# Performance work log

Hardware: AMD Instinct MI355X
Metric: run time of the kernel (lower is better)

The kernel has to match this reference:

```python
import jax, jax.numpy as jnp
import numpy as np

B, N, C, H = 8, 1024, 768, 12
D = C // H
HID = 4 * C
MAX_TEXT_LEN = 512
LN_EPS = 1e-5


def _ln(x, g, b):
    mu = jnp.mean(x, axis=-1, keepdims=True)
    var = jnp.mean(jnp.square(x - mu), axis=-1, keepdims=True)
    return (x - mu) * jax.lax.rsqrt(var + LN_EPS) * g + b


def _mlp(x, w1, b1, w2, b2):
    h = jax.nn.gelu(x @ w1.T + b1, approximate=False)
    return h @ w2.T + b2


def setup_inputs() -> dict:
    key = jax.random.key(0)
    ks = jax.random.split(key, 16)
    s = 0.02
    return {
        "x": jax.random.normal(ks[0], (B, N, C), jnp.float32),
        "mask": jax.random.randint(ks[1], (B, N), 0, 2).astype(bool),
        "rel_bias": jax.random.normal(ks[2], (H, N, N), jnp.float32) * s,
        "w_qkv": jax.random.normal(ks[3], (3 * C, C), jnp.float32) * s,
        "q_bias": jnp.zeros((C,), jnp.float32),
        "v_bias": jnp.zeros((C,), jnp.float32),
        "w_proj": jax.random.normal(ks[4], (C, C), jnp.float32) * s,
        "b_proj": jnp.zeros((C,), jnp.float32),
        "ln1_g": jnp.ones((C,), jnp.float32),
        "ln1_b": jnp.zeros((C,), jnp.float32),
        "ln2t_g": jnp.ones((C,), jnp.float32),
        "ln2t_b": jnp.zeros((C,), jnp.float32),
        "ln2i_g": jnp.ones((C,), jnp.float32),
        "ln2i_b": jnp.zeros((C,), jnp.float32),
        "w1t": jax.random.normal(ks[5], (HID, C), jnp.float32) * s,
        "b1t": jnp.zeros((HID,), jnp.float32),
        "w2t": jax.random.normal(ks[6], (C, HID), jnp.float32) * s,
        "b2t": jnp.zeros((C,), jnp.float32),
        "w1i": jax.random.normal(ks[7], (HID, C), jnp.float32) * s,
        "b1i": jnp.zeros((HID,), jnp.float32),
        "w2i": jax.random.normal(ks[8], (C, HID), jnp.float32) * s,
        "b2i": jnp.zeros((C,), jnp.float32),
        "gamma1": jnp.full((C,), 0.1, jnp.float32),
        "gamma2": jnp.full((C,), 0.1, jnp.float32),
    }


def reference(x, mask, rel_bias, w_qkv, q_bias, v_bias, w_proj, b_proj,
              ln1_g, ln1_b, ln2t_g, ln2t_b, ln2i_g, ln2i_b,
              w1t, b1t, w2t, b2t, w1i, b1i, w2i, b2i, gamma1, gamma2):
    # ---- attention branch ----
    h = _ln(x, ln1_g, ln1_b)
    qkv_bias = jnp.concatenate([q_bias, jnp.zeros_like(v_bias), v_bias])
    qkv = h @ w_qkv.T + qkv_bias                      # [B,N,3C]
    qkv = qkv.reshape(B, N, 3, H, D).transpose(2, 0, 3, 1, 4)  # [3,B,H,N,D]
    q, k, v = qkv[0], qkv[1], qkv[2]
    q = q * (D ** -0.5)
    attn = jnp.einsum('bhnd,bhmd->bhnm',
                      q.astype(jnp.float32), k.astype(jnp.float32))
    attn = attn + rel_bias[None]                      # [B,H,N,N]
    attn = jnp.where(mask[:, None, None, :], attn, -jnp.inf)
    attn = jax.nn.softmax(attn, axis=-1).astype(x.dtype)
    out = jnp.einsum('bhnm,bhmd->bhnd', attn, v)
    out = out.transpose(0, 2, 1, 3).reshape(B, N, C)
    out = out @ w_proj.T + b_proj
    x = x + gamma1 * out
    # ---- dual-branch layer-scaled MLP (mlp_vl is None path) ----
    xt = x[:, :MAX_TEXT_LEN]
    xi = x[:, MAX_TEXT_LEN:]
    xt = xt + gamma2 * _mlp(_ln(xt, ln2t_g, ln2t_b), w1t, b1t, w2t, b2t)
    xi = xi + gamma2 * _mlp(_ln(xi, ln2i_g, ln2i_b), w1i, b1i, w2i, b2i)
    return jnp.concatenate([xt, xi], axis=1)
```

## Files before the change

### kernel.cpp

```cpp
#include <hip/hip_runtime.h>
#include <hip/hip_bf16.h>
#include <math.h>

#define B_    8
#define N_TOK 1024
#define C_    768
#define H_    12
#define D_    64
#define HID_  3072

typedef __attribute__((ext_vector_type(4)))  float f32x4;
typedef __attribute__((ext_vector_type(16))) float f32x16;
typedef __attribute__((ext_vector_type(8)))  short s16x8;
typedef __attribute__((ext_vector_type(4)))  unsigned short u16x4;

static __device__ __forceinline__ unsigned short f2bf(float x){
  union { __hip_bfloat16 h; unsigned short u; } cv;
  cv.h = __float2bfloat16(x);
  return cv.u;
}
static __device__ __forceinline__ float bf2f(unsigned short u){
  return __uint_as_float(((unsigned)u) << 16);
}

#define GLOAD_LDS16(gp, lp) \
  __builtin_amdgcn_global_load_lds((const __attribute__((address_space(1))) unsigned int*)(gp), \
                                   (__attribute__((address_space(3))) unsigned int*)(lp), 16, 0, 0)

__global__ __launch_bounds__(256) void k_cvtall(
    const float* __restrict__ wq,  const float* __restrict__ wp,
    const float* __restrict__ w1t, const float* __restrict__ w2t,
    const float* __restrict__ w1i, const float* __restrict__ w2i,
    const float* __restrict__ bias,
    unsigned short* __restrict__ dq,  unsigned short* __restrict__ dp,
    unsigned short* __restrict__ d1t, unsigned short* __restrict__ d2t,
    unsigned short* __restrict__ d1i, unsigned short* __restrict__ d2i,
    unsigned short* __restrict__ db)
{
  int i = blockIdx.x * 256 + threadIdx.x;
  const float* src; unsigned short* dst; int o;
  if      (i <  442368){ src = wq;  dst = dq;  o = i; }
  else if (i <  589824){ src = wp;  dst = dp;  o = i -  442368; }
  else if (i < 1179648){ src = w1t; dst = d1t; o = i -  589824; }
  else if (i < 1769472){ src = w2t; dst = d2t; o = i - 1179648; }
  else if (i < 2359296){ src = w1i; dst = d1i; o = i - 1769472; }
  else if (i < 2949120){ src = w2i; dst = d2i; o = i - 2359296; }
  else                 { src = bias;dst = db;  o = i - 2949120; }
  float4 v = ((const float4*)src)[o];
  u16x4 r;
  r.x = f2bf(v.x); r.y = f2bf(v.y); r.z = f2bf(v.z); r.w = f2bf(v.w);
  *(u16x4*)(dst + (size_t)o*4) = r;
}

__global__ __launch_bounds__(256) void k_ln1(const float* __restrict__ x,
                                             const float* __restrict__ g,
                                             const float* __restrict__ bta,
                                             unsigned short* __restrict__ out){
  int row  = blockIdx.x*4 + (threadIdx.x >> 6);
  int lane = threadIdx.x & 63;
  const float* xr = x + (size_t)row*C_;
  float v[12]; float s = 0.f;
  #pragma unroll
  for (int i=0;i<12;i++){ v[i] = xr[lane + i*64]; s += v[i]; }
  #pragma unroll
  for (int m=1;m<64;m<<=1) s += __shfl_xor(s, m);
  float mu = s * (1.f/768.f);
  float vs = 0.f;
  #pragma unroll
  for (int i=0;i<12;i++){ float d = v[i]-mu; vs += d*d; }
  #pragma unroll
  for (int m=1;m<64;m<<=1) vs += __shfl_xor(vs, m);
  float rs = rsqrtf(vs*(1.f/768.f) + 1e-5f);
  unsigned short* orow = out + (size_t)row*C_;
  #pragma unroll
  for (int i=0;i<12;i++){ int c = lane + i*64; orow[c] = f2bf((v[i]-mu)*rs*g[c] + bta[c]); }
}

__global__ __launch_bounds__(256) void k_ln2(const float* __restrict__ xmid,
                                             const float* __restrict__ gt, const float* __restrict__ bt,
                                             const float* __restrict__ gi, const float* __restrict__ bi,
                                             unsigned short* __restrict__ outc){
  int row  = blockIdx.x*4 + (threadIdx.x >> 6);
  int lane = threadIdx.x & 63;
  int bb = row >> 10, n = row & 1023;
  const float* G = (n < 512) ? gt : gi;
  const float* Bb = (n < 512) ? bt : bi;
  int crow = (n < 512) ? (bb*512 + n) : (4096 + bb*512 + (n - 512));
  const float* xr = xmid + (size_t)row*C_;
  float v[12]; float s = 0.f;
  #pragma unroll
  for (int i=0;i<12;i++){ v[i] = xr[lane + i*64]; s += v[i]; }
  #pragma unroll
  for (int m=1;m<64;m<<=1) s += __shfl_xor(s, m);
  float mu = s * (1.f/768.f);
  float vs = 0.f;
  #pragma unroll
  for (int i=0;i<12;i++){ float d = v[i]-mu; vs += d*d; }
  #pragma unroll
  for (int m=1;m<64;m<<=1) vs += __shfl_xor(vs, m);
  float rs = rsqrtf(vs*(1.f/768.f) + 1e-5f);
  unsigned short* orow = outc + (size_t)crow*C_;
  #pragma unroll
  for (int i=0;i<12;i++){ int c = lane + i*64; orow[c] = f2bf((v[i]-mu)*rs*G[c] + Bb[c]); }
}

template<int MODE, int TM>
__global__ __launch_bounds__(TM==256 ? 512 : 256, TM==256 ? 2 : 3) void k_gemm2(
    const unsigned short* __restrict__ A,
    const unsigned short* __restrict__ Bw0,
    const unsigned short* __restrict__ Bw1,
    int K,
    const float* __restrict__ bias0,
    const float* __restrict__ bias1,
    const float* __restrict__ qb2,
    const float* __restrict__ resid,
    const float* __restrict__ gamma,
    unsigned short* __restrict__ out_bf,
    float* __restrict__ out_f)
{
  constexpr int THREADS = (TM == 256) ? 512 : 256;
  constexpr int ASLOT = TM * 64;
  constexpr int SLOT  = ASLOT + 8192;
  constexpr int BITS  = 8192 / (THREADS * 16);
  __shared__ __align__(16) char smem[3 * SLOT];
  const int tid = threadIdx.x;
  const int lane = tid & 63, w = tid >> 6;
  const int wr = w >> 1, wc = w & 1;
  const int l31 = lane & 31, h5 = lane >> 5;

  const int gx = gridDim.x, gy = gridDim.y;
  const int nwg = gx * gy;
  const int flat = blockIdx.y * gx + blockIdx.x;
  const int nid = (flat & 7) * (nwg >> 3) + (flat >> 3);
  const int by = nid % gy, bx = nid / gy;
  const int z = blockIdx.z;
  const int row0 = bx*TM, col0 = by*128;

  const unsigned short* Ap = A;
  const unsigned short* Bp = Bw0;
  const float* bias = bias0;
  if (MODE == 2 || MODE == 3){
    if (z){ Ap = A + (size_t)4096*K; Bp = Bw1; bias = bias1; }
  }
  const char* Abase = (const char*)Ap;
  const char* Bbase = (const char*)Bp;
  const size_t rowbytes = (size_t)K*2;
  const int KT2 = K >> 5;

  auto stage = [&](int h, int slot_idx){
    char* slot = smem + slot_idx*SLOT;
    size_t kb = (size_t)h*64;
    #pragma unroll
    for (int it = 0; it < 2; it++){
      int L = it*(THREADS*16) + tid*16;
      int r = L >> 6, cb = L & 63;
      GLOAD_LDS16(Abase + (size_t)(row0 + r)*rowbytes + kb + (cb ^ ((r & 6) << 3)), slot + L);
    }
    #pragma unroll
    for (int it = 0; it < BITS; it++){
      int L = it*(THREADS*16) + tid*16;
      int r = L >> 6, cb = L & 63;
      GLOAD_LDS16(Bbase + (size_t)(col0 + r)*rowbytes + kb + (cb ^ ((r & 6) << 3)), slot + ASLOT + L);
    }
  };

  stage(0, 0); stage(1, 1);
  if constexpr (TM == 256) asm volatile("s_waitcnt vmcnt(3)" ::: "memory");
  else                     asm volatile("s_waitcnt vmcnt(4)" ::: "memory");
  __builtin_amdgcn_s_barrier();

  f32x16 acc[2][2] = {};
  int sh = 2, sc_ = 0;
  for (int h = 0; h < KT2; h++){
    if (h + 2 < KT2){
      stage(h + 2, sh);
      sh = (sh == 2) ? 0 : sh + 1;
    }
    char* slot = smem + sc_*SLOT;
    sc_ = (sc_ == 2) ? 0 : sc_ + 1;
    s16x8 af[2][2], bfr[2][2];
    #pragma unroll
    for (int fm = 0; fm < 2; fm++){
      int ra = wr*64 + fm*32 + l31;
      int swa = (ra & 6) << 3;
      af[fm][0] = *(const s16x8*)(slot + ra*64 + ((h5*16) ^ swa));
      af[fm][1] = *(const s16x8*)(slot + ra*64 + ((32 + h5*16) ^ swa));
    }
    #pragma unroll
    for (int fn = 0; fn < 2; fn++){
      int rb = wc*64 + fn*32 + l31;
      int swb = (rb & 6) << 3;
      bfr[fn][0] = *(const s16x8*)(slot + ASLOT + rb*64 + ((h5*16) ^ swb));
      bfr[fn][1] = *(const s16x8*)(slot + ASLOT + rb*64 + ((32 + h5*16) ^ swb));
    }
    __builtin_amdgcn_s_setprio(1);
    #pragma unroll
    for (int kh = 0; kh < 2; kh++)
      #pragma unroll
      for (int fm = 0; fm < 2; fm++)
        #pragma unroll
        for (int fn = 0; fn < 2; fn++)
          acc[fm][fn] = __builtin_amdgcn_mfma_f32_32x32x16_bf16(af[fm][kh], bfr[fn][kh], acc[fm][fn], 0, 0, 0);
    __builtin_amdgcn_s_setprio(0);
    if (h + 1 < KT2){
      if (h + 2 < KT2){
        if constexpr (TM == 256) asm volatile("s_waitcnt vmcnt(3)" ::: "memory");
        else                     asm volatile("s_waitcnt vmcnt(4)" ::: "memory");
      } else {
        asm volatile("s_waitcnt vmcnt(0)" ::: "memory");
      }
      __builtin_amdgcn_s_barrier();
    }
  }

  #pragma unroll
  for (int fm = 0; fm < 2; fm++){
    #pragma unroll
    for (int fn = 0; fn < 2; fn++){
      int j = col0 + wc*64 + fn*32 + l31;
      f32x16 a = acc[fm][fn];
      if (MODE == 0){
        int which = (j >= 1536) ? 2 : (j >= 768 ? 1 : 0);
        int cj = j - which*768;
        float bs = (which == 0) ? bias0[cj] : (which == 2 ? qb2[cj] : 0.f);
        int head = cj >> 6, d = cj & 63;
        #pragma unroll
        for (int r = 0; r < 16; r++){
          int m = row0 + wr*64 + fm*32 + (r & 3) + 8*(r >> 2) + 4*h5;
          int bb = m >> 10, n = m & 1023;
          float val = a[r] + bs;
          if (which == 0) val *= 0.125f;
          out_bf[((((size_t)which*B_ + bb)*H_ + head)*N_TOK + n)*D_ + d] = f2bf(val);
        }
      } else if (MODE == 1){
        float gm = gamma[j], bs = bias[j];
        #pragma unroll
        for (int r = 0; r < 16; r++){
          int m = row0 + wr*64 + fm*32 + (r & 3) + 8*(r >> 2) + 4*h5;
          size_t idx = (size_t)m*C_ + j;
          out_f[idx] = resid[idx] + gm*(a[r] + bs);
        }
      } else if (MODE == 2){
        float bs = bias[j];
        unsigned short* outp = out_bf + (size_t)z*4096*HID_;
        #pragma unroll
        for (int r = 0; r < 16; r++){
          int m = row0 + wr*64 + fm*32 + (r & 3) + 8*(r >> 2) + 4*h5;
          float t = a[r] + bs;
          outp[(size_t)m*HID_ + j] = f2bf(0.5f*t*(1.f + erff(t*0.70710678118654752f)));
        }
      } else {
        float gm = gamma[j], bs = bias[j];
        #pragma unroll
        for (int r = 0; r < 16; r++){
          int m = row0 + wr*64 + fm*32 + (r & 3) + 8*(r >> 2) + 4*h5;
          int bb = m >> 9, n = (m & 511) + (z ? 512 : 0);
          size_t idx = ((size_t)bb*N_TOK + n)*C_ + j;
          out_f[idx] = resid[idx] + gm*(a[r] + bs);
        }
      }
    }
  }
}

__global__ __launch_bounds__(256, 2) void k_attn(
    const unsigned short* __restrict__ qb,
    const unsigned short* __restrict__ kb,
    const unsigned short* __restrict__ vb,
    const unsigned short* __restrict__ bias_bf,
    const int* __restrict__ mask,
    unsigned short* __restrict__ outb)
{
  __shared__ __align__(16) char smem[45056];
  char* Vt0 = smem;
  char* Vt1 = smem + 8192;
  char* Ks  = smem + 16384;
  char* Bs  = smem + 24576;
  float* maskf = (float*)(smem + 40960);
  char* Oep = smem;

  int wg = blockIdx.x;
  int x = wg & 7, rest = wg >> 3;
  int qt = rest & 7, gl = rest >> 3;
  int g = gl*8 + x;
  int h = g % 12, bb = g / 12;

  const int tid = threadIdx.x, lane = tid & 63, w = tid >> 6;
  const int l31 = lane & 31, h5 = lane >> 5;
  const size_t bh = (size_t)bb*H_ + h;
  const char* qp = (const char*)(qb + bh*N_TOK*D_);
  const char* kp = (const char*)(kb + bh*N_TOK*D_);
  const unsigned short* vp = vb + bh*N_TOK*D_;
  const char* bp = (const char*)(bias_bf + (size_t)h*N_TOK*N_TOK);
  const int q0 = qt*128;
  const int qrow = q0 + w*32 + l31;
  const int qr = w*32 + l31;

  #pragma unroll
  for (int it = 0; it < 2; it++){
    int L = it*4096 + tid*16; int r = L >> 7, cb = L & 127;
    GLOAD_LDS16(kp + (size_t)r*128 + (cb ^ ((r & 7) << 4)), Ks + L);
  }
  #pragma unroll
  for (int it = 0; it < 4; it++){
    int L = it*4096 + tid*16; int r = L >> 7, cb = L & 127;
    GLOAD_LDS16(bp + (size_t)(q0 + r)*2048 + (cb ^ ((r & 7) << 4)), Bs + L);
  }
  unsigned short vv[16];
  #pragma unroll
  for (int j = 0; j < 16; j++) vv[j] = vp[(size_t)(w*16 + j)*D_ + lane];
  {
    int4 m4 = *(const int4*)(mask + bb*N_TOK + tid*4);
    float4 f4;
    f4.x = m4.x ? 0.f : -1e30f; f4.y = m4.y ? 0.f : -1e30f;
    f4.z = m4.z ? 0.f : -1e30f; f4.w = m4.w ? 0.f : -1e30f;
    *(float4*)(maskf + tid*4) = f4;
  }
  s16x8 qf[4];
  #pragma unroll
  for (int t = 0; t < 4; t++)
    qf[t] = *(const s16x8*)(qp + (size_t)qrow*128 + t*32 + h5*16);
  #pragma unroll
  for (int i = 0; i < 2; i++){
    s16x8 pk;
    #pragma unroll
    for (int e = 0; e < 8; e++) pk[e] = (short)vv[i*8 + e];
    *(s16x8*)(Vt0 + lane*128 + ((w*32 + i*16) ^ ((lane & 7) << 4))) = pk;
  }
  __syncthreads();

  f32x16 oacc[2] = {};
  float lrow = 0.f;

  for (int t = 0; t < 16; t++){
    const int kt = t*64;
    char* Vbuf = (t & 1) ? Vt1 : Vt0;
    char* Vnxt = (t & 1) ? Vt0 : Vt1;

    s16x8 kfr[2][4];
    #pragma unroll
    for (int ck = 0; ck < 2; ck++)
      #pragma unroll
      for (int tt = 0; tt < 4; tt++)
        kfr[ck][tt] = *(const s16x8*)(Ks + (ck*32 + l31)*128 + ((tt*32 + h5*16) ^ ((l31 & 7) << 4)));
    u16x4 bv[2][4];
    #pragma unroll
    for (int ck = 0; ck < 2; ck++)
      #pragma unroll
      for (int rq = 0; rq < 4; rq++){
        int off = ck*64 + rq*16 + h5*8;
        bv[ck][rq] = *(const u16x4*)(Bs + qr*128 + (off ^ ((qr & 7) << 4)));
      }
    __syncthreads();

    if (t < 15){
      #pragma unroll
      for (int it = 0; it < 2; it++){
        int L = it*4096 + tid*16; int r = L >> 7, cb = L & 127;
        GLOAD_LDS16(kp + (size_t)(kt + 64 + r)*128 + (cb ^ ((r & 7) << 4)), Ks + L);
      }
      #pragma unroll
      for (int it = 0; it < 4; it++){
        int L = it*4096 + tid*16; int r = L >> 7, cb = L & 127;
        GLOAD_LDS16(bp + (size_t)(q0 + r)*2048 + (size_t)(kt + 64)*2 + (cb ^ ((r & 7) << 4)), Bs + L);
      }
      #pragma unroll
      for (int j = 0; j < 16; j++)
        vv[j] = vp[(size_t)(kt + 64 + w*16 + j)*D_ + lane];
    }

    f32x16 sacc[2] = {};
    __builtin_amdgcn_s_setprio(1);
    #pragma unroll
    for (int tt = 0; tt < 4; tt++){
      sacc[0] = __builtin_amdgcn_mfma_f32_32x32x16_bf16(kfr[0][tt], qf[tt], sacc[0], 0, 0, 0);
      sacc[1] = __builtin_amdgcn_mfma_f32_32x32x16_bf16(kfr[1][tt], qf[tt], sacc[1], 0, 0, 0);
    }
    __builtin_amdgcn_s_setprio(0);

    float sv[2][16];
    float ps = 0.f;
    #pragma unroll
    for (int ck = 0; ck < 2; ck++){
      #pragma unroll
      for (int r = 0; r < 16; r++){
        int kk = ck*32 + (r & 3) + 8*(r >> 2) + 4*h5;
        float p = __expf(sacc[ck][r] + bf2f(bv[ck][r >> 2][r & 3]) + maskf[kt + kk]);
        sv[ck][r] = p;
        ps += p;
      }
    }
    lrow += ps;

    #pragma unroll
    for (int ck = 0; ck < 2; ck++){
      #pragma unroll
      for (int kh = 0; kh < 2; kh++){
        unsigned wA, wB, wC, wD;
        asm("v_cvt_pk_bf16_f32 %0, %1, %2" : "=v"(wA) : "v"(sv[ck][kh*8+0]), "v"(sv[ck][kh*8+1]));
        asm("v_cvt_pk_bf16_f32 %0, %1, %2" : "=v"(wB) : "v"(sv[ck][kh*8+2]), "v"(sv[ck][kh*8+3]));
        asm("v_cvt_pk_bf16_f32 %0, %1, %2" : "=v"(wC) : "v"(sv[ck][kh*8+4]), "v"(sv[ck][kh*8+5]));
        asm("v_cvt_pk_bf16_f32 %0, %1, %2" : "=v"(wD) : "v"(sv[ck][kh*8+6]), "v"(sv[ck][kh*8+7]));
        unsigned tA = (unsigned)__shfl_xor((int)wA, 32);
        unsigned tB = (unsigned)__shfl_xor((int)wB, 32);
        unsigned tC = (unsigned)__shfl_xor((int)wC, 32);
        unsigned tD = (unsigned)__shfl_xor((int)wD, 32);
        union { unsigned u[4]; s16x8 v; } pu;
        pu.u[0] = h5 ? tC : wA;
        pu.u[1] = h5 ? tD : wB;
        pu.u[2] = h5 ? wC : tA;
        pu.u[3] = h5 ? wD : tB;
        __builtin_amdgcn_s_setprio(1);
        #pragma unroll
        for (int dt = 0; dt < 2; dt++){
          int d = dt*32 + l31;
          s16x8 vf = *(const s16x8*)(Vbuf + d*128 + ((ck*64 + kh*32 + h5*16) ^ ((d & 7) << 4)));
          oacc[dt] = __builtin_amdgcn_mfma_f32_32x32x16_bf16(vf, pu.v, oacc[dt], 0, 0, 0);
        }
        __builtin_amdgcn_s_setprio(0);
      }
    }

    if (t < 15){
      #pragma unroll
      for (int i = 0; i < 2; i++){
        s16x8 pk;
        #pragma unroll
        for (int e = 0; e < 8; e++) pk[e] = (short)vv[i*8 + e];
        *(s16x8*)(Vnxt + lane*128 + ((w*32 + i*16) ^ ((lane & 7) << 4))) = pk;
      }
    }
    __syncthreads();
  }

  lrow += __shfl_xor(lrow, 32);
  float inv = 1.f / lrow;
  char* Ow = Oep + w*8192;
  #pragma unroll
  for (int dt = 0; dt < 2; dt++)
    #pragma unroll
    for (int r = 0; r < 16; r++){
      int d = dt*32 + (r & 3) + 8*(r >> 2) + 4*h5;
      *(float*)(Ow + l31*256 + ((d*4) ^ ((l31 & 7) << 4))) = oacc[dt][r] * inv;
    }
  int q2 = lane >> 1, dh = lane & 1;
  float of[32];
  #pragma unroll
  for (int i = 0; i < 8; i++){
    f32x4 v4 = *(const f32x4*)(Ow + q2*256 + ((dh*128 + i*16) ^ ((q2 & 7) << 4)));
    of[i*4+0] = v4[0]; of[i*4+1] = v4[1]; of[i*4+2] = v4[2]; of[i*4+3] = v4[3];
  }
  unsigned short* orow = outb + ((size_t)bb*N_TOK + q0 + w*32 + q2)*C_ + h*64 + dh*32;
  #pragma unroll
  for (int i = 0; i < 4; i++){
    s16x8 ob;
    #pragma unroll
    for (int e = 0; e < 8; e++) ob[e] = (short)f2bf(of[i*8+e]);
    *(s16x8*)(orow + i*8) = ob;
  }
}

extern "C" void kernel_launch(void* const* d_in, const int* in_sizes, int n_in,
                              void* d_out, int out_size, void* d_ws, size_t ws_size,
                              hipStream_t stream) {
  const float* x      = (const float*)d_in[0];
  const int*   mask   = (const int*)  d_in[1];
  const float* relb   = (const float*)d_in[2];
  const float* w_qkv  = (const float*)d_in[3];
  const float* q_bias = (const float*)d_in[4];
  const float* v_bias = (const float*)d_in[5];
  const float* w_proj = (const float*)d_in[6];
  const float* b_proj = (const float*)d_in[7];
  const float* ln1_g  = (const float*)d_in[8];
  const float* ln1_b  = (const float*)d_in[9];
  const float* ln2t_g = (const float*)d_in[10];
  const float* ln2t_b = (const float*)d_in[11];
  const float* ln2i_g = (const float*)d_in[12];
  const float* ln2i_b = (const float*)d_in[13];
  const float* w1t    = (const float*)d_in[14];
  const float* b1t    = (const float*)d_in[15];
  const float* w2t    = (const float*)d_in[16];
  const float* b2t    = (const float*)d_in[17];
  const float* w1i    = (const float*)d_in[18];
  const float* b1i    = (const float*)d_in[19];
  const float* w2i    = (const float*)d_in[20];
  const float* b2i    = (const float*)d_in[21];
  const float* gamma1 = (const float*)d_in[22];
  const float* gamma2 = (const float*)d_in[23];
  float* out = (float*)d_out;
  char* ws = (char*)d_ws;

  size_t off = 0;
  auto nxt = [&](size_t b){ size_t r = off; off += (b + 255) & ~(size_t)255; return r; };
  unsigned short* wq_bf  = (unsigned short*)(ws + nxt((size_t)3*C_*C_*2));
  unsigned short* wp_bf  = (unsigned short*)(ws + nxt((size_t)C_*C_*2));
  unsigned short* w1t_bf = (unsigned short*)(ws + nxt((size_t)HID_*C_*2));
  unsigned short* w2t_bf = (unsigned short*)(ws + nxt((size_t)HID_*C_*2));
  unsigned short* w1i_bf = (unsigned short*)(ws + nxt((size_t)HID_*C_*2));
  unsigned short* w2i_bf = (unsigned short*)(ws + nxt((size_t)HID_*C_*2));
  unsigned short* hln    = (unsigned short*)(ws + nxt((size_t)B_*N_TOK*C_*2));
  unsigned short* qkv    = (unsigned short*)(ws + nxt((size_t)3*B_*N_TOK*C_*2));
  unsigned short* attno  = (unsigned short*)(ws + nxt((size_t)B_*N_TOK*C_*2));
  float*          xmid   = (float*)(ws + nxt((size_t)B_*N_TOK*C_*4));
  unsigned short* ln2c   = hln;
  unsigned short* hidden = qkv;
  unsigned short* bias_bf = (unsigned short*)xmid;

  k_cvtall<<<dim3(23808), 256, 0, stream>>>(w_qkv, w_proj, w1t, w2t, w1i, w2i, relb,
                                            wq_bf, wp_bf, w1t_bf, w2t_bf, w1i_bf, w2i_bf, bias_bf);

  k_ln1<<<dim3(B_*N_TOK/4), 256, 0, stream>>>(x, ln1_g, ln1_b, hln);

  k_gemm2<0,256><<<dim3(32, 18, 1), 512, 0, stream>>>(hln, wq_bf, nullptr, C_,
                                                      q_bias, nullptr, v_bias,
                                                      nullptr, nullptr, qkv, nullptr);

  const size_t qsz = (size_t)B_*H_*N_TOK*D_;
  k_attn<<<dim3(768), 256, 0, stream>>>(qkv, qkv + qsz, qkv + 2*qsz, bias_bf, mask, attno);

  k_gemm2<1,128><<<dim3(64, 6, 1), 256, 0, stream>>>(attno, wp_bf, nullptr, C_,
                                                     b_proj, nullptr, nullptr,
                                                     x, gamma1, nullptr, xmid);

  k_ln2<<<dim3(B_*N_TOK/4), 256, 0, stream>>>(xmid, ln2t_g, ln2t_b, ln2i_g, ln2i_b, ln2c);

  k_gemm2<2,256><<<dim3(16, 24, 2), 512, 0, stream>>>(ln2c, w1t_bf, w1i_bf, C_,
                                                      b1t, b1i, nullptr,
                                                      nullptr, nullptr, hidden, nullptr);

  k_gemm2<3,128><<<dim3(32, 6, 2), 256, 0, stream>>>(hidden, w2t_bf, w2i_bf, HID_,
                                                     b2t, b2i, nullptr,
                                                     xmid, gamma2, nullptr, out);
}
```

Measured before the change: 306.7 us.

## Software-pipeline attention loop: overlap QK of next tile with PV of previous

Restructures the attention inner loop into a two-stage software pipeline. The QK MFMA for tile t+1 is issued before the PV MFMA for tile t, with ping-pong score and bias registers and a triple-buffered V tile in LDS. The goal is to let MFMA work overlap the softmax/exp and LDS latency instead of running them in series. The cost is more LDS (53 KB instead of 45 KB) and higher register pressure, which may lower occupancy under launch_bounds(256,2).

```diff
diff --git a/kernel.cpp b/kernel.cpp
--- a/kernel.cpp
+++ b/kernel.cpp
@@ -271,12 +271,10 @@
     const int* __restrict__ mask,
     unsigned short* __restrict__ outb)
 {
-  __shared__ __align__(16) char smem[45056];
-  char* Vt0 = smem;
-  char* Vt1 = smem + 8192;
-  char* Ks  = smem + 16384;
-  char* Bs  = smem + 24576;
-  float* maskf = (float*)(smem + 40960);
+  __shared__ __align__(16) char smem[53248];
+  char* Ks  = smem + 24576;
+  char* Bs  = smem + 32768;
+  float* maskf = (float*)(smem + 49152);
   char* Oep = smem;
 
   int wg = blockIdx.x;
@@ -296,54 +294,48 @@
   const int qrow = q0 + w*32 + l31;
   const int qr = w*32 + l31;
 
-  #pragma unroll
-  for (int it = 0; it < 2; it++){
-    int L = it*4096 + tid*16; int r = L >> 7, cb = L & 127;
-    GLOAD_LDS16(kp + (size_t)r*128 + (cb ^ ((r & 7) << 4)), Ks + L);
-  }
-  #pragma unroll
-  for (int it = 0; it < 4; it++){
-    int L = it*4096 + tid*16; int r = L >> 7, cb = L & 127;
-    GLOAD_LDS16(bp + (size_t)(q0 + r)*2048 + (cb ^ ((r & 7) << 4)), Bs + L);
-  }
-  unsigned short vv[16];
-  #pragma unroll
-  for (int j = 0; j < 16; j++) vv[j] = vp[(size_t)(w*16 + j)*D_ + lane];
-  {
-    int4 m4 = *(const int4*)(mask + bb*N_TOK + tid*4);
-    float4 f4;
-    f4.x = m4.x ? 0.f : -1e30f; f4.y = m4.y ? 0.f : -1e30f;
-    f4.z = m4.z ? 0.f : -1e30f; f4.w = m4.w ? 0.f : -1e30f;
-    *(float4*)(maskf + tid*4) = f4;
-  }
-  s16x8 qf[4];
-  #pragma unroll
-  for (int t = 0; t < 4; t++)
-    qf[t] = *(const s16x8*)(qp + (size_t)qrow*128 + t*32 + h5*16);
-  #pragma unroll
-  for (int i = 0; i < 2; i++){
-    s16x8 pk;
-    #pragma unroll
-    for (int e = 0; e < 8; e++) pk[e] = (short)vv[i*8 + e];
-    *(s16x8*)(Vt0 + lane*128 + ((w*32 + i*16) ^ ((lane & 7) << 4))) = pk;
-  }
-  __syncthreads();
-
   f32x16 oacc[2] = {};
   float lrow = 0.f;
-
-  for (int t = 0; t < 16; t++){
-    const int kt = t*64;
-    char* Vbuf = (t & 1) ? Vt1 : Vt0;
-    char* Vnxt = (t & 1) ? Vt0 : Vt1;
-
-    s16x8 kfr[2][4];
+  unsigned short vv[16];
+  unsigned puP[16];
+  f32x16 sA[2], sB[2];
+  u16x4 bvA[2][4], bvB[2][4];
+  s16x8 qf[4];
+
+  auto STAGE = [&](int t){
+    size_t kt2 = (size_t)t*128;
+    #pragma unroll
+    for (int it = 0; it < 2; it++){
+      int L = it*4096 + tid*16; int r = L >> 7, cb = L & 127;
+      GLOAD_LDS16(kp + (size_t)(t*64 + r)*128 + (cb ^ ((r & 7) << 4)), Ks + L);
+    }
+    #pragma unroll
+    for (int it = 0; it < 4; it++){
+      int L = it*4096 + tid*16; int r = L >> 7, cb = L & 127;
+      GLOAD_LDS16(bp + (size_t)(q0 + r)*2048 + kt2 + (cb ^ ((r & 7) << 4)), Bs + L);
+    }
+  };
+  auto LOADV = [&](int t){
+    #pragma unroll
+    for (int j = 0; j < 16; j++)
+      vv[j] = vp[(size_t)(t*64 + w*16 + j)*D_ + lane];
+  };
+  auto WRITEV = [&](int t){
+    char* Vn = smem + (t % 3)*8192;
+    #pragma unroll
+    for (int i = 0; i < 2; i++){
+      s16x8 pk;
+      #pragma unroll
+      for (int e = 0; e < 8; e++) pk[e] = (short)vv[i*8 + e];
+      *(s16x8*)(Vn + lane*128 + ((w*32 + i*16) ^ ((lane & 7) << 4))) = pk;
+    }
+  };
+  auto READF = [&](s16x8 (&kf)[2][4], u16x4 (&bv)[2][4]){
     #pragma unroll
     for (int ck = 0; ck < 2; ck++)
       #pragma unroll
       for (int tt = 0; tt < 4; tt++)
-        kfr[ck][tt] = *(const s16x8*)(Ks + (ck*32 + l31)*128 + ((tt*32 + h5*16) ^ ((l31 & 7) << 4)));
-    u16x4 bv[2][4];
+        kf[ck][tt] = *(const s16x8*)(Ks + (ck*32 + l31)*128 + ((tt*32 + h5*16) ^ ((l31 & 7) << 4)));
     #pragma unroll
     for (int ck = 0; ck < 2; ck++)
       #pragma unroll
@@ -351,33 +343,19 @@
         int off = ck*64 + rq*16 + h5*8;
         bv[ck][rq] = *(const u16x4*)(Bs + qr*128 + (off ^ ((qr & 7) << 4)));
       }
-    __syncthreads();
-
-    if (t < 15){
-      #pragma unroll
-      for (int it = 0; it < 2; it++){
-        int L = it*4096 + tid*16; int r = L >> 7, cb = L & 127;
-        GLOAD_LDS16(kp + (size_t)(kt + 64 + r)*128 + (cb ^ ((r & 7) << 4)), Ks + L);
-      }
-      #pragma unroll
-      for (int it = 0; it < 4; it++){
-        int L = it*4096 + tid*16; int r = L >> 7, cb = L & 127;
-        GLOAD_LDS16(bp + (size_t)(q0 + r)*2048 + (size_t)(kt + 64)*2 + (cb ^ ((r & 7) << 4)), Bs + L);
-      }
-      #pragma unroll
-      for (int j = 0; j < 16; j++)
-        vv[j] = vp[(size_t)(kt + 64 + w*16 + j)*D_ + lane];
-    }
-
-    f32x16 sacc[2] = {};
+  };
+  auto QK = [&](s16x8 (&kf)[2][4], f32x16* sc){
+    sc[0] = (f32x16){};
+    sc[1] = (f32x16){};
     __builtin_amdgcn_s_setprio(1);
     #pragma unroll
     for (int tt = 0; tt < 4; tt++){
-      sacc[0] = __builtin_amdgcn_mfma_f32_32x32x16_bf16(kfr[0][tt], qf[tt], sacc[0], 0, 0, 0);
-      sacc[1] = __builtin_amdgcn_mfma_f32_32x32x16_bf16(kfr[1][tt], qf[tt], sacc[1], 0, 0, 0);
+      sc[0] = __builtin_amdgcn_mfma_f32_32x32x16_bf16(kf[0][tt], qf[tt], sc[0], 0, 0, 0);
+      sc[1] = __builtin_amdgcn_mfma_f32_32x32x16_bf16(kf[1][tt], qf[tt], sc[1], 0, 0, 0);
     }
     __builtin_amdgcn_s_setprio(0);
-
+  };
+  auto SOFTPACK = [&](f32x16* sc, u16x4 (&bv)[2][4], int kt){
     float sv[2][16];
     float ps = 0.f;
     #pragma unroll
@@ -385,13 +363,12 @@
       #pragma unroll
       for (int r = 0; r < 16; r++){
         int kk = ck*32 + (r & 3) + 8*(r >> 2) + 4*h5;
-        float p = __expf(sacc[ck][r] + bf2f(bv[ck][r >> 2][r & 3]) + maskf[kt + kk]);
+        float p = __expf(sc[ck][r] + bf2f(bv[ck][r >> 2][r & 3]) + maskf[kt + kk]);
         sv[ck][r] = p;
         ps += p;
       }
     }
     lrow += ps;
-
     #pragma unroll
     for (int ck = 0; ck < 2; ck++){
       #pragma unroll
@@ -405,33 +382,86 @@
         unsigned tB = (unsigned)__shfl_xor((int)wB, 32);
         unsigned tC = (unsigned)__shfl_xor((int)wC, 32);
         unsigned tD = (unsigned)__shfl_xor((int)wD, 32);
+        int base = (ck*2 + kh)*4;
+        puP[base+0] = h5 ? tC : wA;
+        puP[base+1] = h5 ? tD : wB;
+        puP[base+2] = h5 ? wC : tA;
+        puP[base+3] = h5 ? wD : tB;
+      }
+    }
+  };
+  auto PV = [&](int t){
+    char* Vbuf = smem + (t % 3)*8192;
+    __builtin_amdgcn_s_setprio(1);
+    #pragma unroll
+    for (int ck = 0; ck < 2; ck++){
+      #pragma unroll
+      for (int kh = 0; kh < 2; kh++){
         union { unsigned u[4]; s16x8 v; } pu;
-        pu.u[0] = h5 ? tC : wA;
-        pu.u[1] = h5 ? tD : wB;
-        pu.u[2] = h5 ? wC : tA;
-        pu.u[3] = h5 ? wD : tB;
-        __builtin_amdgcn_s_setprio(1);
+        int base = (ck*2 + kh)*4;
+        pu.u[0] = puP[base+0]; pu.u[1] = puP[base+1];
+        pu.u[2] = puP[base+2]; pu.u[3] = puP[base+3];
         #pragma unroll
         for (int dt = 0; dt < 2; dt++){
           int d = dt*32 + l31;
           s16x8 vf = *(const s16x8*)(Vbuf + d*128 + ((ck*64 + kh*32 + h5*16) ^ ((d & 7) << 4)));
           oacc[dt] = __builtin_amdgcn_mfma_f32_32x32x16_bf16(vf, pu.v, oacc[dt], 0, 0, 0);
         }
-        __builtin_amdgcn_s_setprio(0);
       }
     }
-
-    if (t < 15){
-      #pragma unroll
-      for (int i = 0; i < 2; i++){
-        s16x8 pk;
-        #pragma unroll
-        for (int e = 0; e < 8; e++) pk[e] = (short)vv[i*8 + e];
-        *(s16x8*)(Vnxt + lane*128 + ((w*32 + i*16) ^ ((lane & 7) << 4))) = pk;
-      }
-    }
+    __builtin_amdgcn_s_setprio(0);
+  };
+
+  STAGE(0);
+  LOADV(0);
+  {
+    int4 m4 = *(const int4*)(mask + bb*N_TOK + tid*4);
+    float4 f4;
+    f4.x = m4.x ? 0.f : -1e30f; f4.y = m4.y ? 0.f : -1e30f;
+    f4.z = m4.z ? 0.f : -1e30f; f4.w = m4.w ? 0.f : -1e30f;
+    *(float4*)(maskf + tid*4) = f4;
+  }
+  #pragma unroll
+  for (int t = 0; t < 4; t++)
+    qf[t] = *(const s16x8*)(qp + (size_t)qrow*128 + t*32 + h5*16);
+  WRITEV(0);
+  __syncthreads();
+  {
+    s16x8 kfr[2][4];
+    READF(kfr, bvA);
     __syncthreads();
-  }
+    STAGE(1);
+    LOADV(1);
+    QK(kfr, sA);
+  }
+
+  for (int tp = 0; tp < 8; tp++){
+    const int t0 = tp*2, t1 = tp*2 + 1;
+    if (t0 > 0) PV(t0 - 1);
+    SOFTPACK(sA, bvA, t0*64);
+    {
+      WRITEV(t0 + 1);
+      __syncthreads();
+      s16x8 kfr[2][4];
+      READF(kfr, bvB);
+      __syncthreads();
+      if (t0 + 2 < 16){ STAGE(t0 + 2); LOADV(t0 + 2); }
+      QK(kfr, sB);
+    }
+    PV(t1 - 1);
+    SOFTPACK(sB, bvB, t1*64);
+    if (t1 < 15){
+      WRITEV(t1 + 1);
+      __syncthreads();
+      s16x8 kfr[2][4];
+      READF(kfr, bvA);
+      __syncthreads();
+      if (t1 + 2 < 16){ STAGE(t1 + 2); LOADV(t1 + 2); }
+      QK(kfr, sA);
+    }
+  }
+  PV(15);
+  __syncthreads();
 
   lrow += __shfl_xor(lrow, 32);
   float inv = 1.f / lrow;
```

Result: slower. 407.2 us (+32.8%).
